# Kernel tuning notes

Measured on AMD Instinct MI355X. Metric: run time of the kernel, lower is better.

## Reference

```python
import jax, jax.numpy as jnp
import numpy as np

NEG_FILL = -9e15  # matches torch.full(..., -9000000000000000.0)
LRELU_ALPHA = 0.2


def setup_inputs() -> dict:
    key = jax.random.key(0)
    k1, k2, k3, k4, k5 = jax.random.split(key, 5)
    N, IN_DIM, OUT_DIM = 50000, 256, 128
    T, E = 4096, 262144
    features = jax.random.normal(k1, (N, IN_DIM), dtype=jnp.float32)
    adj = jax.random.randint(k2, (2, E), 0, N, dtype=jnp.int64)
    target_index_out = jax.random.randint(k3, (E,), 0, T, dtype=jnp.int64)
    # xavier_uniform-ish scale for params
    W = jax.random.normal(k4, (IN_DIM, OUT_DIM), dtype=jnp.float32) * (1.414 * np.sqrt(2.0 / (IN_DIM + OUT_DIM)))
    a = jax.random.normal(k5, (2 * OUT_DIM, 1), dtype=jnp.float32) * (1.414 * np.sqrt(2.0 / (2 * OUT_DIM + 1)))
    return {
        "features": features,
        "adj": adj,
        "target_index_out": target_index_out,
        "W": W,
        "a": a,
        "target_len": T,
        "neighbor_len": N,
    }


def reference(features, adj, target_index_out, W, a, target_len, neighbor_len):
    # h: [N, out_dim]
    h = features @ W
    out_dim = h.shape[1]
    # edge scores: cat([h[src], h[dst]]) @ a == h[src] @ a[:d] + h[dst] @ a[d:]
    # (identical math, avoids materializing the [E, 2d] concat)
    e_src = h[adj[0]] @ a[:out_dim, 0]  # [E]
    e_dst = h[adj[1]] @ a[out_dim:, 0]  # [E]
    e = jax.nn.leaky_relu(e_src + e_dst, negative_slope=LRELU_ALPHA)
    # matching torch advanced-indexing assignment)
    attention = jnp.full((target_len, neighbor_len), NEG_FILL, dtype=h.dtype)
    attention = attention.at[target_index_out, adj[1]].set(e, mode="drop")
    attention = jax.nn.softmax(attention, axis=1)
    # dropout with p=0.0 / eval mode: identity
    h_prime = attention @ h  # [T, out_dim]
    return jax.nn.elu(h_prime)
```

## Files before the change

kernel.cpp:

```cpp
#include <hip/hip_runtime.h>
#include <hip/hip_bf16.h>
#include <hip/hip_fp16.h>
#include <cstdint>

#define IN_DIM 256
#define OUT_DIM 128
#define CAP 192

typedef __attribute__((ext_vector_type(8))) short short8;
typedef __attribute__((ext_vector_type(4))) float f32x4;

__device__ __forceinline__ unsigned short f2bf(float f) {
    __hip_bfloat16 b = __float2bfloat16(f);
    return *reinterpret_cast<unsigned short*>(&b);
}
__device__ __forceinline__ float bf2f(unsigned short u) {
    union { unsigned int i; float f; } v;
    v.i = ((unsigned int)u) << 16;
    return v.f;
}

__device__ __forceinline__ void gload16(const void* g, void* l) {
    __builtin_amdgcn_global_load_lds(
        (const __attribute__((address_space(1))) void*)g,
        (__attribute__((address_space(3))) void*)l, 16, 0, 0);
}

__global__ __launch_bounds__(256) void wt_kernel(const float* __restrict__ Wm,
                                                 unsigned short* __restrict__ Wt,
                                                 int* __restrict__ cursor, int T) {
    const int idx = blockIdx.x * 256 + threadIdx.x;
    const int k = idx >> 7;
    const int n = idx & 127;
    Wt[n * 256 + k] = f2bf(Wm[idx]);
    if (idx < T) cursor[idx] = 0;
}

__global__ __launch_bounds__(256, 4) void gemm_h(const float* __restrict__ A,
                                                 const unsigned short* __restrict__ Wt,
                                                 const float* __restrict__ av,
                                                 unsigned short* __restrict__ Hb,
                                                 float* __restrict__ s1,
                                                 float* __restrict__ s2, int Nn) {
    __shared__ char As[2][8192];
    __shared__ char Bs[2][8192];
    const int tid  = threadIdx.x;
    const int lane = tid & 63;
    const int w    = tid >> 6;
    const int wm = w >> 1, wn = w & 1;
    const int l15 = lane & 15;
    const int lhi = lane >> 4;
    const int bm  = blockIdx.x * 64;
    const char* Ab = (const char*)A;
    const char* Wb = (const char*)Wt;

    f32x4 acc[2][4];
    #pragma unroll
    for (int i = 0; i < 2; ++i)
        #pragma unroll
        for (int j = 0; j < 4; ++j) acc[i][j] = (f32x4){0.f, 0.f, 0.f, 0.f};

    auto stage = [&](int buf, int t) {
        const int k0 = t * 32;
        #pragma unroll
        for (int i = 0; i < 2; ++i) {
            const int rbase = i * 32 + w * 8;
            const int rl = rbase + (lane >> 3);
            int gr = bm + rl; if (gr >= Nn) gr = Nn - 1;
            const int osw = ((lane & 7) * 16) ^ ((rl & 7) << 4);
            gload16(Ab + (size_t)gr * 1024 + (size_t)k0 * 4 + osw,
                    &As[buf][rbase * 128]);
        }
        #pragma unroll
        for (int i = 0; i < 2; ++i) {
            const int nbase = i * 64 + w * 16;
            const int nl = nbase + (lane >> 2);
            const int osw = ((lane & 3) * 16) ^ ((((nl ^ (nl >> 2)) & 3)) << 4);
            gload16(Wb + (size_t)nl * 512 + (size_t)k0 * 2 + osw,
                    &Bs[buf][nbase * 64]);
        }
    };

    auto compute = [&](int buf) {
        short8 af[2], bf4[4];
        #pragma unroll
        for (int i = 0; i < 2; ++i) {
            const int rl = wm * 32 + i * 16 + l15;
            const int sw = (rl & 7) << 4;
            const int ob = lhi * 32;
            const float4 lo = *(const float4*)&As[buf][rl * 128 + (ob ^ sw)];
            const float4 hi = *(const float4*)&As[buf][rl * 128 + ((ob + 16) ^ sw)];
            short8 a;
            a[0] = (short)f2bf(lo.x); a[1] = (short)f2bf(lo.y);
            a[2] = (short)f2bf(lo.z); a[3] = (short)f2bf(lo.w);
            a[4] = (short)f2bf(hi.x); a[5] = (short)f2bf(hi.y);
            a[6] = (short)f2bf(hi.z); a[7] = (short)f2bf(hi.w);
            af[i] = a;
        }
        #pragma unroll
        for (int j = 0; j < 4; ++j) {
            const int nl = wn * 64 + j * 16 + l15;
            const int ob = lhi * 16;
            const int sw = ((nl ^ (nl >> 2)) & 3) << 4;
            bf4[j] = *(const short8*)&Bs[buf][nl * 64 + (ob ^ sw)];
        }
        #pragma unroll
        for (int i = 0; i < 2; ++i)
            #pragma unroll
            for (int j = 0; j < 4; ++j)
                acc[i][j] = __builtin_amdgcn_mfma_f32_16x16x32_bf16(af[i], bf4[j], acc[i][j], 0, 0, 0);
    };

    stage(0, 0);
    __syncthreads();
    #pragma unroll
    for (int t = 0; t < 8; ++t) {
        if (t < 7) stage((t + 1) & 1, t + 1);
        compute(t & 1);
        __syncthreads();
    }

    float* sc = (float*)&As[0][0];
    #pragma unroll
    for (int i = 0; i < 2; ++i) {
        #pragma unroll
        for (int r = 0; r < 4; ++r) {
            const int rl  = wm * 32 + i * 16 + lhi * 4 + r;
            const int row = bm + rl;
            if (row < Nn) {
                float p1 = 0.f, p2 = 0.f;
                #pragma unroll
                for (int j = 0; j < 4; ++j) {
                    const int col = wn * 64 + j * 16 + l15;
                    const float v = acc[i][j][r];
                    Hb[(size_t)row * OUT_DIM + col] = f2bf(v);
                    p1 = fmaf(v, av[col], p1);
                    p2 = fmaf(v, av[128 + col], p2);
                }
                #pragma unroll
                for (int o = 1; o < 16; o <<= 1) {
                    p1 += __shfl_xor(p1, o);
                    p2 += __shfl_xor(p2, o);
                }
                if (l15 == 0) {
                    sc[wn * 64 + rl]       = p1;
                    sc[128 + wn * 64 + rl] = p2;
                }
            }
        }
    }
    __syncthreads();
    if (tid < 64) {
        const int gr = bm + tid;
        if (gr < Nn) {
            s1[gr] = sc[tid] + sc[64 + tid];
            s2[gr] = sc[128 + tid] + sc[192 + tid];
        }
    }
}

__global__ __launch_bounds__(256) void scatter_kernel(const int* __restrict__ tio,
                                                      const int* __restrict__ adj,
                                                      const float* __restrict__ s1,
                                                      const float* __restrict__ s2,
                                                      int* __restrict__ cursor,
                                                      uint2* __restrict__ e2, int E) {
    const int k = blockIdx.x * 256 + threadIdx.x;
    if (k >= E) return;
    const int t   = tio[k];
    const int src = adj[k];
    const int dst = adj[E + k];
    float ev = s1[src] + s2[dst];
    ev = ev > 0.f ? ev : 0.2f * ev;
    const unsigned short sh = __half_as_ushort(__float2half(ev));
    const int pos = atomicAdd(&cursor[t], 1);
    if (pos < CAP) {
        e2[(size_t)t * CAP + pos] = make_uint2((unsigned)k,
                                               (unsigned)dst | ((unsigned)sh << 16));
    }
}

__device__ __forceinline__ void fma8(float* a, float p, uint4 v) {
    a[0] = fmaf(p, bf2f((unsigned short)(v.x)),       a[0]);
    a[1] = fmaf(p, bf2f((unsigned short)(v.x >> 16)), a[1]);
    a[2] = fmaf(p, bf2f((unsigned short)(v.y)),       a[2]);
    a[3] = fmaf(p, bf2f((unsigned short)(v.y >> 16)), a[3]);
    a[4] = fmaf(p, bf2f((unsigned short)(v.z)),       a[4]);
    a[5] = fmaf(p, bf2f((unsigned short)(v.z >> 16)), a[5]);
    a[6] = fmaf(p, bf2f((unsigned short)(v.w)),       a[6]);
    a[7] = fmaf(p, bf2f((unsigned short)(v.w >> 16)), a[7]);
}

__global__ __launch_bounds__(256) void row_kernel(const int* __restrict__ cursor,
                                                  const uint2* __restrict__ e2,
                                                  const unsigned short* __restrict__ Hb,
                                                  float* __restrict__ out, int Nn) {
    __shared__ int   sh_dst[CAP];
    __shared__ int   sh_kk[CAP];
    __shared__ float sh_p[CAP];
    __shared__ float psum[16][128];
    __shared__ float red[4];
    const int row  = blockIdx.x;
    const int tid  = threadIdx.x;
    const int lane = tid & 63;
    const int wave = tid >> 6;
    const int grp  = tid >> 4;
    const int slot = tid & 15;
    int cnt = cursor[row];
    if (cnt > CAP) cnt = CAP;
    const size_t base = (size_t)row * CAP;

    for (int i = tid; i < cnt; i += 256) {
        const uint2 v = e2[base + i];
        sh_kk[i]  = (int)v.x;
        sh_dst[i] = (int)(v.y & 0xffffu);
        sh_p[i]   = __half2float(__ushort_as_half((unsigned short)(v.y >> 16)));
    }
    __syncthreads();

    uint4 vv[8];
    if (cnt > 0) {
        #pragma unroll
        for (int u = 0; u < 8; ++u) {
            const int j = grp + u * 16;
            const int d = sh_dst[(j < cnt) ? j : 0];
            vv[u] = *(const uint4*)(Hb + (size_t)d * OUT_DIM + slot * 8);
        }
        float ls = 0.f;
        for (int i = tid; i < cnt; i += 256) {
            const int dst = sh_dst[i];
            const int kk  = sh_kk[i];
            bool act = true;
            for (int j2 = 0; j2 < cnt; ++j2)
                if (sh_dst[j2] == dst && sh_kk[j2] > kk) { act = false; break; }
            const float p = act ? __expf(sh_p[i]) : 0.f;
            sh_p[i] = p;
            ls += p;
        }
        #pragma unroll
        for (int o = 32; o; o >>= 1) ls += __shfl_xor(ls, o);
        if (lane == 0) red[wave] = ls;
    }
    __syncthreads();

    float acc8[8];
    #pragma unroll
    for (int d = 0; d < 8; ++d) acc8[d] = 0.f;
    float inv = 0.f;
    if (cnt > 0) {
        const float ls = red[0] + red[1] + red[2] + red[3];
        inv = (ls > 0.f) ? 1.f / ls : 0.f;
        #pragma unroll
        for (int u = 0; u < 8; ++u) {
            const int j = grp + u * 16;
            const float p = (j < cnt) ? sh_p[j] : 0.f;
            fma8(acc8, p, vv[u]);
        }
        for (int j = grp + 128; j < cnt; j += 16) {
            const uint4 v0 = *(const uint4*)(Hb + (size_t)sh_dst[j] * OUT_DIM + slot * 8);
            fma8(acc8, sh_p[j], v0);
        }
    }
    *(float4*)&psum[grp][slot * 8]     = make_float4(acc8[0], acc8[1], acc8[2], acc8[3]);
    *(float4*)&psum[grp][slot * 8 + 4] = make_float4(acc8[4], acc8[5], acc8[6], acc8[7]);
    __syncthreads();

    if (tid < 128) {
        float v = 0.f;
        #pragma unroll
        for (int k2 = 0; k2 < 16; ++k2) v += psum[k2][tid];
        v *= inv;
        if (cnt == 0) {
            float t = 0.f;
            for (int n = 0; n < Nn; ++n) t += bf2f(Hb[(size_t)n * OUT_DIM + tid]);
            v = t / (float)Nn;
        }
        v = v > 0.f ? v : expm1f(v);
        out[(size_t)row * OUT_DIM + tid] = v;
    }
}

extern "C" void kernel_launch(void* const* d_in, const int* in_sizes, int n_in,
                              void* d_out, int out_size, void* d_ws, size_t ws_size,
                              hipStream_t stream) {
    const float* features = (const float*)d_in[0];
    const int*   adj      = (const int*)d_in[1];
    const int*   tio      = (const int*)d_in[2];
    const float* Wm       = (const float*)d_in[3];
    const float* av       = (const float*)d_in[4];
    float* out = (float*)d_out;

    const int N = in_sizes[0] / IN_DIM;
    const int E = in_sizes[2];
    const int T = out_size / OUT_DIM;

    char* ws = (char*)d_ws;
    unsigned short* Hb = (unsigned short*)ws; ws += (size_t)N * OUT_DIM * 2;
    unsigned short* Wt = (unsigned short*)ws; ws += (size_t)IN_DIM * OUT_DIM * 2;
    float* s1 = (float*)ws;                   ws += (size_t)N * 4;
    float* s2 = (float*)ws;                   ws += (size_t)N * 4;
    int* cursor = (int*)ws;                   ws += (size_t)T * 4;
    uint2* e2 = (uint2*)ws;                   ws += (size_t)T * CAP * 8;

    wt_kernel<<<(IN_DIM * OUT_DIM) / 256, 256, 0, stream>>>(Wm, Wt, cursor, T);
    gemm_h<<<(N + 63) / 64, 256, 0, stream>>>(features, Wt, av, Hb, s1, s2, N);
    scatter_kernel<<<(E + 255) / 256, 256, 0, stream>>>(tio, adj, s1, s2, cursor, e2, E);
    row_kernel<<<T, 256, 0, stream>>>(cursor, e2, Hb, out, N);
}
```

Before: 83.75 us.

## Fuse scatter and row kernels into persistent kernel with grid barrier

Merges the edge-scatter kernel and the per-row softmax/aggregation kernel into one persistent kernel. A grid-stride loop does the scatter, a global atomic counter acts as a grid-wide barrier, and then the blocks loop over target rows. This removes one kernel launch and its gap, and sizes the grid from occupancy (capped at 2048 blocks). The barrier relies on every block being co-resident, so it can deadlock if occupancy is misreported. The fused kernel may also run with lower occupancy in the row phase.

```diff
diff --git a/kernel.cpp b/kernel.cpp
--- a/kernel.cpp
+++ b/kernel.cpp
@@ -28,12 +28,14 @@
 
 __global__ __launch_bounds__(256) void wt_kernel(const float* __restrict__ Wm,
                                                  unsigned short* __restrict__ Wt,
-                                                 int* __restrict__ cursor, int T) {
+                                                 int* __restrict__ cursor,
+                                                 int* __restrict__ done, int T) {
     const int idx = blockIdx.x * 256 + threadIdx.x;
     const int k = idx >> 7;
     const int n = idx & 127;
     Wt[n * 256 + k] = f2bf(Wm[idx]);
     if (idx < T) cursor[idx] = 0;
+    if (idx == 0) *done = 0;
 }
 
 __global__ __launch_bounds__(256, 4) void gemm_h(const float* __restrict__ A,
@@ -159,27 +161,6 @@
     }
 }
 
-__global__ __launch_bounds__(256) void scatter_kernel(const int* __restrict__ tio,
-                                                      const int* __restrict__ adj,
-                                                      const float* __restrict__ s1,
-                                                      const float* __restrict__ s2,
-                                                      int* __restrict__ cursor,
-                                                      uint2* __restrict__ e2, int E) {
-    const int k = blockIdx.x * 256 + threadIdx.x;
-    if (k >= E) return;
-    const int t   = tio[k];
-    const int src = adj[k];
-    const int dst = adj[E + k];
-    float ev = s1[src] + s2[dst];
-    ev = ev > 0.f ? ev : 0.2f * ev;
-    const unsigned short sh = __half_as_ushort(__float2half(ev));
-    const int pos = atomicAdd(&cursor[t], 1);
-    if (pos < CAP) {
-        e2[(size_t)t * CAP + pos] = make_uint2((unsigned)k,
-                                               (unsigned)dst | ((unsigned)sh << 16));
-    }
-}
-
 __device__ __forceinline__ void fma8(float* a, float p, uint4 v) {
     a[0] = fmaf(p, bf2f((unsigned short)(v.x)),       a[0]);
     a[1] = fmaf(p, bf2f((unsigned short)(v.x >> 16)), a[1]);
@@ -191,92 +172,130 @@
     a[7] = fmaf(p, bf2f((unsigned short)(v.w >> 16)), a[7]);
 }
 
-__global__ __launch_bounds__(256) void row_kernel(const int* __restrict__ cursor,
-                                                  const uint2* __restrict__ e2,
-                                                  const unsigned short* __restrict__ Hb,
-                                                  float* __restrict__ out, int Nn) {
+__global__ __launch_bounds__(256) void scatter_row(const int* __restrict__ tio,
+                                                   const int* __restrict__ adj,
+                                                   const float* __restrict__ s1,
+                                                   const float* __restrict__ s2,
+                                                   int* __restrict__ cursor,
+                                                   uint2* __restrict__ e2,
+                                                   const unsigned short* __restrict__ Hb,
+                                                   float* __restrict__ out,
+                                                   int* __restrict__ done,
+                                                   int E, int T, int Nn, int G) {
     __shared__ int   sh_dst[CAP];
     __shared__ int   sh_kk[CAP];
     __shared__ float sh_p[CAP];
     __shared__ float psum[16][128];
     __shared__ float red[4];
-    const int row  = blockIdx.x;
     const int tid  = threadIdx.x;
+    const int bid  = blockIdx.x;
+    const int gid  = bid * 256 + tid;
+    const int GT   = G * 256;
     const int lane = tid & 63;
     const int wave = tid >> 6;
     const int grp  = tid >> 4;
     const int slot = tid & 15;
-    int cnt = cursor[row];
-    if (cnt > CAP) cnt = CAP;
-    const size_t base = (size_t)row * CAP;
-
-    for (int i = tid; i < cnt; i += 256) {
-        const uint2 v = e2[base + i];
-        sh_kk[i]  = (int)v.x;
-        sh_dst[i] = (int)(v.y & 0xffffu);
-        sh_p[i]   = __half2float(__ushort_as_half((unsigned short)(v.y >> 16)));
-    }
+
+    for (int k = gid; k < E; k += GT) {
+        const int t   = tio[k];
+        const int src = adj[k];
+        const int dst = adj[E + k];
+        float ev = s1[src] + s2[dst];
+        ev = ev > 0.f ? ev : 0.2f * ev;
+        const unsigned short sh = __half_as_ushort(__float2half(ev));
+        const int pos = atomicAdd(&cursor[t], 1);
+        if (pos < CAP) {
+            e2[(size_t)t * CAP + pos] = make_uint2((unsigned)k,
+                                                   (unsigned)dst | ((unsigned)sh << 16));
+        }
+    }
+
+    __threadfence();
     __syncthreads();
-
-    uint4 vv[8];
-    if (cnt > 0) {
-        #pragma unroll
-        for (int u = 0; u < 8; ++u) {
-            const int j = grp + u * 16;
-            const int d = sh_dst[(j < cnt) ? j : 0];
-            vv[u] = *(const uint4*)(Hb + (size_t)d * OUT_DIM + slot * 8);
-        }
-        float ls = 0.f;
+    if (tid == 0) {
+        __hip_atomic_fetch_add(done, 1, __ATOMIC_RELEASE, __HIP_MEMORY_SCOPE_AGENT);
+        while (__hip_atomic_load(done, __ATOMIC_ACQUIRE, __HIP_MEMORY_SCOPE_AGENT) < G)
+            __builtin_amdgcn_s_sleep(8);
+    }
+    __syncthreads();
+
+    for (int row = bid; row < T; row += G) {
+        int cnt = __hip_atomic_load(&cursor[row], __ATOMIC_RELAXED, __HIP_MEMORY_SCOPE_AGENT);
+        if (cnt > CAP) cnt = CAP;
+        const size_t base = (size_t)row * CAP;
+
         for (int i = tid; i < cnt; i += 256) {
-            const int dst = sh_dst[i];
-            const int kk  = sh_kk[i];
-            bool act = true;
-            for (int j2 = 0; j2 < cnt; ++j2)
-                if (sh_dst[j2] == dst && sh_kk[j2] > kk) { act = false; break; }
-            const float p = act ? __expf(sh_p[i]) : 0.f;
-            sh_p[i] = p;
-            ls += p;
-        }
-        #pragma unroll
-        for (int o = 32; o; o >>= 1) ls += __shfl_xor(ls, o);
-        if (lane == 0) red[wave] = ls;
-    }
-    __syncthreads();
-
-    float acc8[8];
-    #pragma unroll
-    for (int d = 0; d < 8; ++d) acc8[d] = 0.f;
-    float inv = 0.f;
-    if (cnt > 0) {
-        const float ls = red[0] + red[1] + red[2] + red[3];
-        inv = (ls > 0.f) ? 1.f / ls : 0.f;
-        #pragma unroll
-        for (int u = 0; u < 8; ++u) {
-            const int j = grp + u * 16;
-            const float p = (j < cnt) ? sh_p[j] : 0.f;
-            fma8(acc8, p, vv[u]);
-        }
-        for (int j = grp + 128; j < cnt; j += 16) {
-            const uint4 v0 = *(const uint4*)(Hb + (size_t)sh_dst[j] * OUT_DIM + slot * 8);
-            fma8(acc8, sh_p[j], v0);
-        }
-    }
-    *(float4*)&psum[grp][slot * 8]     = make_float4(acc8[0], acc8[1], acc8[2], acc8[3]);
-    *(float4*)&psum[grp][slot * 8 + 4] = make_float4(acc8[4], acc8[5], acc8[6], acc8[7]);
-    __syncthreads();
-
-    if (tid < 128) {
-        float v = 0.f;
-        #pragma unroll
-        for (int k2 = 0; k2 < 16; ++k2) v += psum[k2][tid];
-        v *= inv;
-        if (cnt == 0) {
-            float t = 0.f;
-            for (int n = 0; n < Nn; ++n) t += bf2f(Hb[(size_t)n * OUT_DIM + tid]);
-            v = t / (float)Nn;
-        }
-        v = v > 0.f ? v : expm1f(v);
-        out[(size_t)row * OUT_DIM + tid] = v;
+            const unsigned long long vl = __hip_atomic_load(
+                (const unsigned long long*)&e2[base + i],
+                __ATOMIC_RELAXED, __HIP_MEMORY_SCOPE_AGENT);
+            sh_kk[i]  = (int)(unsigned)(vl & 0xffffffffull);
+            const unsigned y = (unsigned)(vl >> 32);
+            sh_dst[i] = (int)(y & 0xffffu);
+            sh_p[i]   = __half2float(__ushort_as_half((unsigned short)(y >> 16)));
+        }
+        __syncthreads();
+
+        uint4 vv[8];
+        if (cnt > 0) {
+            #pragma unroll
+            for (int u = 0; u < 8; ++u) {
+                const int j = grp + u * 16;
+                const int d = sh_dst[(j < cnt) ? j : 0];
+                vv[u] = *(const uint4*)(Hb + (size_t)d * OUT_DIM + slot * 8);
+            }
+            float ls = 0.f;
+            for (int i = tid; i < cnt; i += 256) {
+                const int dst = sh_dst[i];
+                const int kk  = sh_kk[i];
+                bool act = true;
+                for (int j2 = 0; j2 < cnt; ++j2)
+                    if (sh_dst[j2] == dst && sh_kk[j2] > kk) { act = false; break; }
+                const float p = act ? __expf(sh_p[i]) : 0.f;
+                sh_p[i] = p;
+                ls += p;
+            }
+            #pragma unroll
+            for (int o = 32; o; o >>= 1) ls += __shfl_xor(ls, o);
+            if (lane == 0) red[wave] = ls;
+        }
+        __syncthreads();
+
+        float acc8[8];
+        #pragma unroll
+        for (int d = 0; d < 8; ++d) acc8[d] = 0.f;
+        float inv = 0.f;
+        if (cnt > 0) {
+            const float ls = red[0] + red[1] + red[2] + red[3];
+            inv = (ls > 0.f) ? 1.f / ls : 0.f;
+            #pragma unroll
+            for (int u = 0; u < 8; ++u) {
+                const int j = grp + u * 16;
+                const float p = (j < cnt) ? sh_p[j] : 0.f;
+                fma8(acc8, p, vv[u]);
+            }
+            for (int j = grp + 128; j < cnt; j += 16) {
+                const uint4 v0 = *(const uint4*)(Hb + (size_t)sh_dst[j] * OUT_DIM + slot * 8);
+                fma8(acc8, sh_p[j], v0);
+            }
+        }
+        *(float4*)&psum[grp][slot * 8]     = make_float4(acc8[0], acc8[1], acc8[2], acc8[3]);
+        *(float4*)&psum[grp][slot * 8 + 4] = make_float4(acc8[4], acc8[5], acc8[6], acc8[7]);
+        __syncthreads();
+
+        if (tid < 128) {
+            float v = 0.f;
+            #pragma unroll
+            for (int k2 = 0; k2 < 16; ++k2) v += psum[k2][tid];
+            v *= inv;
+            if (cnt == 0) {
+                float t = 0.f;
+                for (int n = 0; n < Nn; ++n) t += bf2f(Hb[(size_t)n * OUT_DIM + tid]);
+                v = t / (float)Nn;
+            }
+            v = v > 0.f ? v : expm1f(v);
+            out[(size_t)row * OUT_DIM + tid] = v;
+        }
+        __syncthreads();
     }
 }
 
@@ -300,10 +319,17 @@
     float* s1 = (float*)ws;                   ws += (size_t)N * 4;
     float* s2 = (float*)ws;                   ws += (size_t)N * 4;
     int* cursor = (int*)ws;                   ws += (size_t)T * 4;
+    int* done = (int*)ws;                     ws += 256;
     uint2* e2 = (uint2*)ws;                   ws += (size_t)T * CAP * 8;
 
-    wt_kernel<<<(IN_DIM * OUT_DIM) / 256, 256, 0, stream>>>(Wm, Wt, cursor, T);
+    int occ = 0;
+    (void)hipOccupancyMaxActiveBlocksPerMultiprocessor(&occ, (const void*)scatter_row, 256, 0);
+    if (occ < 1) occ = 4;
+    long long g = (long long)occ * 256;
+    if (g > 2048) g = 2048;
+    const int G = (int)g;
+
+    wt_kernel<<<(IN_DIM * OUT_DIM) / 256, 256, 0, stream>>>(Wm, Wt, cursor, done, T);
     gemm_h<<<(N + 63) / 64, 256, 0, stream>>>(features, Wt, av, Hb, s1, s2, N);
-    scatter_kernel<<<(E + 255) / 256, 256, 0, stream>>>(tio, adj, s1, s2, cursor, e2, E);
-    row_kernel<<<T, 256, 0, stream>>>(cursor, e2, Hb, out, N);
-}
+    scatter_row<<<G, 256, 0, stream>>>(tio, adj, s1, s2, cursor, e2, Hb, out, done, E, T, N, G);
+}
```

After: 250.7 us. 199% more time.
